# Performance work log

Measured on AMD Instinct MI355X. Metric: run time of the kernel, lower is better.

## Reference

```python
import jax, jax.numpy as jnp
import numpy as np

N = 50000      # nodes
E = 600000     # edges
D = 128        # dim_h == num_features
G = 512        # graphs in batch
BN_EPS = 1e-5


def _w(k, shape, fan_in):
    return jax.random.normal(k, shape, jnp.float32) * np.float32(1.0 / np.sqrt(fan_in))


def setup_inputs() -> dict:
    key = jax.random.key(0)
    ks = jax.random.split(key, 16)
    return {
        "x": jax.random.normal(ks[0], (N, D), jnp.float32),
        "edge_index": jax.random.randint(ks[1], (2, E), 0, N, jnp.int64),
        "batch": jnp.sort(jax.random.randint(ks[2], (N,), 0, G, jnp.int64)),
        # GINConv 1 MLP: Linear -> BN -> ReLU -> Linear -> ReLU
        "c1_W1": _w(ks[3], (D, D), D), "c1_b1": jnp.zeros((D,), jnp.float32),
        "c1_g": jnp.ones((D,), jnp.float32), "c1_be": jnp.zeros((D,), jnp.float32),
        "c1_W2": _w(ks[4], (D, D), D), "c1_b2": jnp.zeros((D,), jnp.float32),
        # GINConv 2 MLP
        "c2_W1": _w(ks[5], (D, D), D), "c2_b1": jnp.zeros((D,), jnp.float32),
        "c2_g": jnp.ones((D,), jnp.float32), "c2_be": jnp.zeros((D,), jnp.float32),
        "c2_W2": _w(ks[6], (D, D), D), "c2_b2": jnp.zeros((D,), jnp.float32),
        # readout MLP
        "lin1_W": _w(ks[7], (4 * D, 4 * D), 4 * D), "lin1_b": jnp.zeros((4 * D,), jnp.float32),
        "lin2_W": _w(ks[8], (4 * D, 1), 4 * D), "lin2_b": jnp.zeros((1,), jnp.float32),
    }


def _gin_conv(x, src, dst, W1, b1, g, be, W2, b2):
    # sum aggregation of neighbor messages (PyG GINConv, eps=0)
    agg = jax.ops.segment_sum(x[src], dst, num_segments=x.shape[0])
    h = (agg + x) @ W1 + b1
    # BatchNorm1d, training mode (biased batch stats over nodes)
    mu = h.mean(axis=0)
    var = h.var(axis=0)
    h = jax.nn.relu(g * (h - mu) * jax.lax.rsqrt(var + BN_EPS) + be)
    return jax.nn.relu(h @ W2 + b2)


def _pool(h, batch):
    add = jax.ops.segment_sum(h, batch, num_segments=G)
    mx = jax.ops.segment_max(h, batch, num_segments=G)
    mx = jnp.where(jnp.isfinite(mx), mx, 0.0)  # empty segments -> 0
    return add, mx


def reference(x, edge_index, batch,
              c1_W1, c1_b1, c1_g, c1_be, c1_W2, c1_b2,
              c2_W1, c2_b1, c2_g, c2_be, c2_W2, c2_b2,
              lin1_W, lin1_b, lin2_W, lin2_b):
    src, dst = edge_index[0], edge_index[1]
    h1 = _gin_conv(x, src, dst, c1_W1, c1_b1, c1_g, c1_be, c1_W2, c1_b2)
    h2 = _gin_conv(h1, src, dst, c2_W1, c2_b1, c2_g, c2_be, c2_W2, c2_b2)
    a1, m1 = _pool(h1, batch)
    a2, m2 = _pool(h2, batch)
    h = jnp.concatenate([a1, a2, m1, m2], axis=1)  # [G, 4D]
    h = jax.nn.relu(h @ lin1_W + lin1_b)
    h = h @ lin2_W + lin2_b  # [G, 1]
    return jax.nn.sigmoid(h), h
```

## Files before the change

### kernel.cpp

```cpp
#include <hip/hip_runtime.h>

#define D 128
#define GNUM 512

typedef _Float16 f16;
typedef _Float16 f16x2 __attribute__((ext_vector_type(2)));
typedef _Float16 f16x8 __attribute__((ext_vector_type(8)));
typedef float f32x4 __attribute__((ext_vector_type(4)));

__global__ void deg_kernel(const int* __restrict__ ei, int* __restrict__ deg,
                           int nE) {
  int e = blockIdx.x * blockDim.x + threadIdx.x;
  if (e < nE) atomicAdd(&deg[ei[nE + e]], 1);
}

__global__ __launch_bounds__(256) void partial_kernel(
    const int* __restrict__ deg, int* __restrict__ partials, int n) {
  __shared__ int sh[256];
  const int t = threadIdx.x;
  const int i = blockIdx.x * 512 + t * 2;
  int s = 0;
  if (i < n) s += deg[i];
  if (i + 1 < n) s += deg[i + 1];
  sh[t] = s;
  __syncthreads();
#pragma unroll
  for (int off = 128; off > 0; off >>= 1) {
    if (t < off) sh[t] += sh[t + off];
    __syncthreads();
  }
  if (t == 0) partials[blockIdx.x] = sh[0];
}

__global__ __launch_bounds__(128) void scanp_kernel(
    int* __restrict__ partials, int nP, int* __restrict__ rowptr, int n,
    int nE) {
  __shared__ int sh[128];
  const int t = threadIdx.x;
  const int v = (t < nP) ? partials[t] : 0;
  sh[t] = v;
  __syncthreads();
#pragma unroll
  for (int off = 1; off < 128; off <<= 1) {
    int u = (t >= off) ? sh[t - off] : 0;
    __syncthreads();
    sh[t] += u;
    __syncthreads();
  }
  if (t < nP) partials[t] = sh[t] - v;
  if (t == 0) rowptr[n] = nE;
}

__global__ __launch_bounds__(256) void emit_kernel(
    const int* __restrict__ deg, const int* __restrict__ partials,
    int* __restrict__ rowptr, int* __restrict__ cursor, int n) {
  __shared__ int sh[256];
  const int t = threadIdx.x;
  const int i = blockIdx.x * 512 + t * 2;
  const int d0 = (i < n) ? deg[i] : 0;
  const int d1 = (i + 1 < n) ? deg[i + 1] : 0;
  const int s = d0 + d1;
  sh[t] = s;
  __syncthreads();
#pragma unroll
  for (int off = 1; off < 256; off <<= 1) {
    int u = (t >= off) ? sh[t - off] : 0;
    __syncthreads();
    sh[t] += u;
    __syncthreads();
  }
  int base = partials[blockIdx.x] + sh[t] - s;
  if (i < n) {
    rowptr[i] = base;
    cursor[i] = base;
    base += d0;
  }
  if (i + 1 < n) {
    rowptr[i + 1] = base;
    cursor[i + 1] = base;
  }
}

__global__ void fill_kernel(const int* __restrict__ ei, int* __restrict__ cursor,
                            int* __restrict__ csr, int nE) {
  int e = blockIdx.x * blockDim.x + threadIdx.x;
  if (e < nE) {
    int d = ei[nE + e];
    int pos = atomicAdd(&cursor[d], 1);
    csr[pos] = ei[e];
  }
}

__global__ __launch_bounds__(256) void prep_kernel(
    const float* __restrict__ x, f16* __restrict__ x16, int n4,
    const float* __restrict__ W0, const float* __restrict__ W1,
    const float* __restrict__ W2, const float* __restrict__ W3,
    f16* __restrict__ wt, const int* __restrict__ batch,
    int* __restrict__ gstart, int n, int nxblk) {
  const int b = blockIdx.x;
  if (b < nxblk) {
    int i = b * 256 + threadIdx.x;
    if (i < n4) {
      float4 v = ((const float4*)x)[i];
      union { f16 h[4]; uint2 u; } p;
      p.h[0] = (f16)v.x; p.h[1] = (f16)v.y;
      p.h[2] = (f16)v.z; p.h[3] = (f16)v.w;
      ((uint2*)x16)[i] = p.u;
    }
  } else if (b < nxblk + 256) {
    int idx = (b - nxblk) * 256 + threadIdx.x;
    int wsel = idx >> 14;
    int rem = idx & 16383;
    int col = rem >> 7, k = rem & 127;
    const float* W = (wsel == 0) ? W0 : (wsel == 1) ? W1
                                      : (wsel == 2) ? W2 : W3;
    wt[idx] = (f16)W[k * D + col];
  } else {
    int g = (b - nxblk - 256) * 256 + threadIdx.x;
    if (g > GNUM) return;
    if (g == GNUM) { gstart[g] = n; return; }
    int lo = 0, hi = n;
    while (lo < hi) {
      int mid = (lo + hi) >> 1;
      if (batch[mid] < g) lo = mid + 1; else hi = mid;
    }
    gstart[g] = lo;
  }
}

__global__ __launch_bounds__(256) void gemmfused_kernel(
    const f16* __restrict__ feat, const int* __restrict__ rowptr,
    const int* __restrict__ csr, const f16* __restrict__ WT,
    const float* __restrict__ bias, f16* __restrict__ C,
    float* __restrict__ pstat, int n) {
  __shared__ f16 alds[32][136];
  const int t = threadIdx.x;
  const int w = t >> 6;
  const int l = t & 63;
  const int rb = blockIdx.x * 32;

  {
    const int c = l * 2;
#pragma unroll 1
    for (int rr = w * 8; rr < w * 8 + 8; rr++) {
      const int row = rb + rr;
      float a0 = 0.f, a1 = 0.f;
      if (row < n) {
        f16x2 v = *(const f16x2*)(feat + (size_t)row * D + c);
        a0 = (float)v[0]; a1 = (float)v[1];
        const int beg = rowptr[row], end = rowptr[row + 1];
        int i = beg;
        for (; i + 7 < end; i += 8) {
          int s0 = csr[i],     s1 = csr[i + 1], s2 = csr[i + 2], s3 = csr[i + 3];
          int s4 = csr[i + 4], s5 = csr[i + 5], s6 = csr[i + 6], s7 = csr[i + 7];
          f16x2 v0 = *(const f16x2*)(feat + (size_t)s0 * D + c);
          f16x2 v1 = *(const f16x2*)(feat + (size_t)s1 * D + c);
          f16x2 v2 = *(const f16x2*)(feat + (size_t)s2 * D + c);
          f16x2 v3 = *(const f16x2*)(feat + (size_t)s3 * D + c);
          f16x2 v4 = *(const f16x2*)(feat + (size_t)s4 * D + c);
          f16x2 v5 = *(const f16x2*)(feat + (size_t)s5 * D + c);
          f16x2 v6 = *(const f16x2*)(feat + (size_t)s6 * D + c);
          f16x2 v7 = *(const f16x2*)(feat + (size_t)s7 * D + c);
          a0 += ((float)v0[0] + (float)v1[0]) + ((float)v2[0] + (float)v3[0]) +
                ((float)v4[0] + (float)v5[0]) + ((float)v6[0] + (float)v7[0]);
          a1 += ((float)v0[1] + (float)v1[1]) + ((float)v2[1] + (float)v3[1]) +
                ((float)v4[1] + (float)v5[1]) + ((float)v6[1] + (float)v7[1]);
        }
        for (; i + 3 < end; i += 4) {
          int s0 = csr[i], s1 = csr[i + 1], s2 = csr[i + 2], s3 = csr[i + 3];
          f16x2 v0 = *(const f16x2*)(feat + (size_t)s0 * D + c);
          f16x2 v1 = *(const f16x2*)(feat + (size_t)s1 * D + c);
          f16x2 v2 = *(const f16x2*)(feat + (size_t)s2 * D + c);
          f16x2 v3 = *(const f16x2*)(feat + (size_t)s3 * D + c);
          a0 += (float)v0[0] + (float)v1[0] + (float)v2[0] + (float)v3[0];
          a1 += (float)v0[1] + (float)v1[1] + (float)v2[1] + (float)v3[1];
        }
        for (; i < end; i++) {
          f16x2 v = *(const f16x2*)(feat + (size_t)csr[i] * D + c);
          a0 += (float)v[0];
          a1 += (float)v[1];
        }
      }
      f16x2 o;
      o[0] = (f16)a0;
      o[1] = (f16)a1;
      *(f16x2*)(&alds[rr][c]) = o;
    }
  }
  __syncthreads();

  const int lr = l & 15;
  const int lq = l >> 4;
  const int lk = lq * 8;
  const int cb = w * 32;

  f32x4 acc[2][2];
#pragma unroll
  for (int m = 0; m < 2; m++)
#pragma unroll
    for (int nt = 0; nt < 2; nt++) acc[m][nt] = (f32x4)0.f;

#pragma unroll
  for (int s = 0; s < 4; s++) {
    const int k = s * 32 + lk;
    f16x8 af[2];
#pragma unroll
    for (int m = 0; m < 2; m++)
      af[m] = *(const f16x8*)(&alds[m * 16 + lr][k]);
    f16x8 bf[2];
#pragma unroll
    for (int nt = 0; nt < 2; nt++)
      bf[nt] = *(const f16x8*)(WT + (size_t)(cb + nt * 16 + lr) * D + k);
#pragma unroll
    for (int m = 0; m < 2; m++)
#pragma unroll
      for (int nt = 0; nt < 2; nt++)
        acc[m][nt] = __builtin_amdgcn_mfma_f32_16x16x32_f16(af[m], bf[nt],
                                                            acc[m][nt], 0, 0, 0);
  }

  float ts[2], tq[2];
#pragma unroll
  for (int nt = 0; nt < 2; nt++) { ts[nt] = 0.f; tq[nt] = 0.f; }
#pragma unroll
  for (int m = 0; m < 2; m++)
#pragma unroll
    for (int r = 0; r < 4; r++) {
      int row = rb + m * 16 + lq * 4 + r;
      if (row < n) {
#pragma unroll
        for (int nt = 0; nt < 2; nt++) {
          float v = acc[m][nt][r] + bias[cb + nt * 16 + lr];
          C[(size_t)row * D + cb + nt * 16 + lr] = (f16)v;
          ts[nt] += v;
          tq[nt] = fmaf(v, v, tq[nt]);
        }
      }
    }
#pragma unroll
  for (int nt = 0; nt < 2; nt++) {
    ts[nt] += __shfl_xor(ts[nt], 16); ts[nt] += __shfl_xor(ts[nt], 32);
    tq[nt] += __shfl_xor(tq[nt], 16); tq[nt] += __shfl_xor(tq[nt], 32);
  }
  if (l < 16) {
    float* ps = pstat + (size_t)blockIdx.x * 256;
#pragma unroll
    for (int nt = 0; nt < 2; nt++) {
      ps[cb + nt * 16 + l] = ts[nt];
      ps[128 + cb + nt * 16 + l] = tq[nt];
    }
  }
}

__global__ __launch_bounds__(64) void gemmbn_kernel(
    const f16* __restrict__ A, const float* __restrict__ ss,
    const f16* __restrict__ WT, const float* __restrict__ bias,
    f16* __restrict__ C, int n) {
  const int l = threadIdx.x;
  const int rw0 = blockIdx.x * 32;
  const int lr = l & 15;
  const int lq = l >> 4;
  const int lk = lq * 8;

  f32x4 acc[2][8];
#pragma unroll
  for (int m = 0; m < 2; m++)
#pragma unroll
    for (int nt = 0; nt < 8; nt++) acc[m][nt] = (f32x4)0.f;

#pragma unroll
  for (int s = 0; s < 4; s++) {
    const int k = s * 32 + lk;
    float4 c0 = *(const float4*)(ss + k);
    float4 c1 = *(const float4*)(ss + k + 4);
    float4 h0 = *(const float4*)(ss + 128 + k);
    float4 h1 = *(const float4*)(ss + 128 + k + 4);
    f16x8 af[2];
#pragma unroll
    for (int m = 0; m < 2; m++) {
      int row = rw0 + m * 16 + lr;
      f16x8 v = (f16x8)(f16)0.f;
      if (row < n) v = *(const f16x8*)(A + (size_t)row * D + k);
      f16x8 r;
      r[0] = (f16)fmaxf(0.f, fmaf((float)v[0], c0.x, h0.x));
      r[1] = (f16)fmaxf(0.f, fmaf((float)v[1], c0.y, h0.y));
      r[2] = (f16)fmaxf(0.f, fmaf((float)v[2], c0.z, h0.z));
      r[3] = (f16)fmaxf(0.f, fmaf((float)v[3], c0.w, h0.w));
      r[4] = (f16)fmaxf(0.f, fmaf((float)v[4], c1.x, h1.x));
      r[5] = (f16)fmaxf(0.f, fmaf((float)v[5], c1.y, h1.y));
      r[6] = (f16)fmaxf(0.f, fmaf((float)v[6], c1.z, h1.z));
      r[7] = (f16)fmaxf(0.f, fmaf((float)v[7], c1.w, h1.w));
      af[m] = r;
    }
    f16x8 bf[8];
#pragma unroll
    for (int nt = 0; nt < 8; nt++)
      bf[nt] = *(const f16x8*)(WT + (size_t)(nt * 16 + lr) * D + k);
#pragma unroll
    for (int m = 0; m < 2; m++)
#pragma unroll
      for (int nt = 0; nt < 8; nt++)
        acc[m][nt] = __builtin_amdgcn_mfma_f32_16x16x32_f16(af[m], bf[nt],
                                                            acc[m][nt], 0, 0, 0);
  }

#pragma unroll
  for (int m = 0; m < 2; m++)
#pragma unroll
    for (int r = 0; r < 4; r++) {
      int row = rw0 + m * 16 + lq * 4 + r;
      if (row < n) {
#pragma unroll
        for (int nt = 0; nt < 8; nt++) {
          float v = fmaxf(0.f, acc[m][nt][r] + bias[nt * 16 + lr]);
          C[(size_t)row * D + nt * 16 + lr] = (f16)v;
        }
      }
    }
}

__global__ __launch_bounds__(256) void statreduce_kernel(
    const float* __restrict__ pstat, float* __restrict__ pstat2, int nB) {
  int c = threadIdx.x;
  float s = 0.f;
  for (int b = blockIdx.x; b < nB; b += 32)
    s += pstat[(size_t)b * 256 + c];
  pstat2[(size_t)blockIdx.x * 256 + c] = s;
}

__global__ void bnstats_kernel(const float* __restrict__ pstat2,
                               const float* __restrict__ g,
                               const float* __restrict__ be,
                               float* __restrict__ ss, int n) {
  int c = threadIdx.x;
  float s = 0.f, sq = 0.f;
#pragma unroll
  for (int i = 0; i < 32; i++) {
    s += pstat2[i * 256 + c];
    sq += pstat2[i * 256 + 128 + c];
  }
  float inv_n = 1.0f / (float)n;
  float mean = s * inv_n;
  float var = sq * inv_n - mean * mean;
  float scale = g[c] * rsqrtf(var + 1e-5f);
  ss[c] = scale;
  ss[128 + c] = be[c] - mean * scale;
}

__global__ __launch_bounds__(512) void poolout_kernel(
    const f16* __restrict__ h1, const f16* __restrict__ h2,
    const int* __restrict__ gstart, const float* __restrict__ W1,
    const float* __restrict__ b1, const float* __restrict__ W2,
    const float* __restrict__ b2, float* __restrict__ out) {
  __shared__ float prow[2][512];
  __shared__ float shred[8][2];
  const int t = threadIdx.x;
  const int g0 = blockIdx.x * 2;
  {
    const int sub = t >> 8;
    const int src = (t >> 7) & 1;
    const int c = t & 127;
    const f16* hp = src ? h2 : h1;
    const int r0 = gstart[g0 + sub], r1 = gstart[g0 + sub + 1];
    float s = 0.f, m = 0.f;
    int r = r0;
    for (; r + 1 < r1; r += 2) {
      float a = (float)hp[(size_t)r * D + c];
      float b = (float)hp[(size_t)(r + 1) * D + c];
      s += a + b;
      m = fmaxf(m, fmaxf(a, b));
    }
    if (r < r1) {
      float a = (float)hp[(size_t)r * D + c];
      s += a;
      m = fmaxf(m, a);
    }
    prow[sub][src * 128 + c] = s;
    prow[sub][256 + src * 128 + c] = m;
  }
  __syncthreads();
  float a00 = 0.f, a01 = 0.f, a10 = 0.f, a11 = 0.f;
  for (int k = 0; k < 512; k += 2) {
    float w0 = W1[(size_t)k * 512 + t];
    float w1 = W1[(size_t)(k + 1) * 512 + t];
    a00 = fmaf(prow[0][k], w0, a00);
    a01 = fmaf(prow[0][k + 1], w1, a01);
    a10 = fmaf(prow[1][k], w0, a10);
    a11 = fmaf(prow[1][k + 1], w1, a11);
  }
  const float bj = b1[t];
  const float w2 = W2[t];
  float acc0 = fmaxf(0.f, a00 + a01 + bj) * w2;
  float acc1 = fmaxf(0.f, a10 + a11 + bj) * w2;
  const int w = t >> 6, l = t & 63;
#pragma unroll
  for (int off = 32; off > 0; off >>= 1) {
    acc0 += __shfl_down(acc0, off);
    acc1 += __shfl_down(acc1, off);
  }
  if (l == 0) {
    shred[w][0] = acc0;
    shred[w][1] = acc1;
  }
  __syncthreads();
  if (t < 2) {
    float s = 0.f;
#pragma unroll
    for (int i = 0; i < 8; i++) s += shred[i][t];
    float h = s + b2[0];
    out[g0 + t] = 1.0f / (1.0f + expf(-h));
    out[GNUM + g0 + t] = h;
  }
}

extern "C" void kernel_launch(void* const* d_in, const int* in_sizes, int n_in,
                              void* d_out, int out_size, void* d_ws,
                              size_t ws_size, hipStream_t stream) {
  const float* x = (const float*)d_in[0];
  const int* ei = (const int*)d_in[1];
  const int* batch = (const int*)d_in[2];
  const float* c1_W1 = (const float*)d_in[3];
  const float* c1_b1 = (const float*)d_in[4];
  const float* c1_g  = (const float*)d_in[5];
  const float* c1_be = (const float*)d_in[6];
  const float* c1_W2 = (const float*)d_in[7];
  const float* c1_b2 = (const float*)d_in[8];
  const float* c2_W1 = (const float*)d_in[9];
  const float* c2_b1 = (const float*)d_in[10];
  const float* c2_g  = (const float*)d_in[11];
  const float* c2_be = (const float*)d_in[12];
  const float* c2_W2 = (const float*)d_in[13];
  const float* c2_b2 = (const float*)d_in[14];
  const float* lin1_W = (const float*)d_in[15];
  const float* lin1_b = (const float*)d_in[16];
  const float* lin2_W = (const float*)d_in[17];
  const float* lin2_b = (const float*)d_in[18];

  const int n = in_sizes[0] / D;
  const int nE = in_sizes[1] / 2;

  char* p = (char*)d_ws;
  auto take = [&](size_t bytes) {
    char* r = p;
    p += (bytes + 255) & ~(size_t)255;
    return r;
  };
  f16*   hpre   = (f16*)take((size_t)n * D * 2);
  f16*   h2buf  = (f16*)take((size_t)n * D * 2);
  f16*   h1     = (f16*)take((size_t)n * D * 2);
  f16*   wt     = (f16*)take(4 * 16384 * 2);
  int*   deg    = (int*)take((size_t)n * 4);
  float* ssbuf  = (float*)take(256 * 4);
  int*   gstart = (int*)take((GNUM + 1) * 4);
  int* rowptr   = (int*)take((size_t)(n + 1) * 4);
  int* cursor   = (int*)take((size_t)(n + 1) * 4);
  int* partials = (int*)take(128 * 4);
  int* csr      = (int*)take((size_t)nE * 4);
  const int nB = (n + 31) / 32;
  float* pstat  = (float*)take((size_t)nB * 256 * 4);
  float* pstat2 = (float*)take(32 * 256 * 4);

  const int edge_grid = (nE + 255) / 256;
  const int nP = (n + 511) / 512;
  const int n4 = n * D / 4;
  const int nxblk = (n4 + 255) / 256;
  const int prep_grid = nxblk + 256 + 3;

  hipMemsetAsync(deg, 0, (size_t)n * sizeof(int), stream);
  deg_kernel<<<edge_grid, 256, 0, stream>>>(ei, deg, nE);
  partial_kernel<<<nP, 256, 0, stream>>>(deg, partials, n);
  scanp_kernel<<<1, 128, 0, stream>>>(partials, nP, rowptr, n, nE);
  emit_kernel<<<nP, 256, 0, stream>>>(deg, partials, rowptr, cursor, n);
  fill_kernel<<<edge_grid, 256, 0, stream>>>(ei, cursor, csr, nE);
  prep_kernel<<<prep_grid, 256, 0, stream>>>(x, h1, n4, c1_W1, c1_W2, c2_W1,
                                             c2_W2, wt, batch, gstart, n,
                                             nxblk);

  gemmfused_kernel<<<nB, 256, 0, stream>>>(h1, rowptr, csr, wt, c1_b1, hpre,
                                           pstat, n);
  statreduce_kernel<<<32, 256, 0, stream>>>(pstat, pstat2, nB);
  bnstats_kernel<<<1, 128, 0, stream>>>(pstat2, c1_g, c1_be, ssbuf, n);
  gemmbn_kernel<<<nB, 64, 0, stream>>>(hpre, ssbuf, wt + 16384, c1_b2, h1, n);

  gemmfused_kernel<<<nB, 256, 0, stream>>>(h1, rowptr, csr, wt + 32768, c2_b1,
                                           hpre, pstat, n);
  statreduce_kernel<<<32, 256, 0, stream>>>(pstat, pstat2, nB);
  bnstats_kernel<<<1, 128, 0, stream>>>(pstat2, c2_g, c2_be, ssbuf, n);
  gemmbn_kernel<<<nB, 64, 0, stream>>>(hpre, ssbuf, wt + 49152, c2_b2,
                                       h2buf, n);

  poolout_kernel<<<GNUM / 2, 512, 0, stream>>>(h1, h2buf, gstart, lin1_W,
                                               lin1_b, lin2_W, lin2_b,
                                               (float*)d_out);
}
```

Baseline: 254.6 us.

## Fold degree count into prep kernel and reduce BN stats with atomics

The degree-counting pass moves into the prep kernel as extra blocks, so one launch does the x conversion, weight transpose, graph starts and degree atomics. The gemmfused kernel now atomically adds its per-block column sums into 32 striped partial buffers instead of writing per-block partials. This removes the two statreduce launches and the large pstat buffer, and a single memset now zeroes deg and both stat buffers. The cost is float atomic contention and a non-deterministic summation order for the batch-norm statistics.

```diff
diff --git a/kernel.cpp b/kernel.cpp
--- a/kernel.cpp
+++ b/kernel.cpp
@@ -7,12 +7,6 @@
 typedef _Float16 f16x2 __attribute__((ext_vector_type(2)));
 typedef _Float16 f16x8 __attribute__((ext_vector_type(8)));
 typedef float f32x4 __attribute__((ext_vector_type(4)));
-
-__global__ void deg_kernel(const int* __restrict__ ei, int* __restrict__ deg,
-                           int nE) {
-  int e = blockIdx.x * blockDim.x + threadIdx.x;
-  if (e < nE) atomicAdd(&deg[ei[nE + e]], 1);
-}
 
 __global__ __launch_bounds__(256) void partial_kernel(
     const int* __restrict__ deg, int* __restrict__ partials, int n) {
@@ -96,7 +90,8 @@
     const float* __restrict__ W0, const float* __restrict__ W1,
     const float* __restrict__ W2, const float* __restrict__ W3,
     f16* __restrict__ wt, const int* __restrict__ batch,
-    int* __restrict__ gstart, int n, int nxblk) {
+    int* __restrict__ gstart, const int* __restrict__ ei,
+    int* __restrict__ deg, int nE, int n, int nxblk) {
   const int b = blockIdx.x;
   if (b < nxblk) {
     int i = b * 256 + threadIdx.x;
@@ -115,7 +110,7 @@
     const float* W = (wsel == 0) ? W0 : (wsel == 1) ? W1
                                       : (wsel == 2) ? W2 : W3;
     wt[idx] = (f16)W[k * D + col];
-  } else {
+  } else if (b < nxblk + 259) {
     int g = (b - nxblk - 256) * 256 + threadIdx.x;
     if (g > GNUM) return;
     if (g == GNUM) { gstart[g] = n; return; }
@@ -125,6 +120,9 @@
       if (batch[mid] < g) lo = mid + 1; else hi = mid;
     }
     gstart[g] = lo;
+  } else {
+    int e = (b - nxblk - 259) * 256 + threadIdx.x;
+    if (e < nE) atomicAdd(&deg[ei[nE + e]], 1);
   }
 }
 
@@ -132,7 +130,7 @@
     const f16* __restrict__ feat, const int* __restrict__ rowptr,
     const int* __restrict__ csr, const f16* __restrict__ WT,
     const float* __restrict__ bias, f16* __restrict__ C,
-    float* __restrict__ pstat, int n) {
+    float* __restrict__ pstat2, int n) {
   __shared__ f16 alds[32][136];
   const int t = threadIdx.x;
   const int w = t >> 6;
@@ -243,11 +241,11 @@
     tq[nt] += __shfl_xor(tq[nt], 16); tq[nt] += __shfl_xor(tq[nt], 32);
   }
   if (l < 16) {
-    float* ps = pstat + (size_t)blockIdx.x * 256;
+    float* ps = pstat2 + (size_t)(blockIdx.x & 31) * 256;
 #pragma unroll
     for (int nt = 0; nt < 2; nt++) {
-      ps[cb + nt * 16 + l] = ts[nt];
-      ps[128 + cb + nt * 16 + l] = tq[nt];
+      atomicAdd(ps + cb + nt * 16 + l, ts[nt]);
+      atomicAdd(ps + 128 + cb + nt * 16 + l, tq[nt]);
     }
   }
 }
@@ -317,15 +315,6 @@
         }
       }
     }
-}
-
-__global__ __launch_bounds__(256) void statreduce_kernel(
-    const float* __restrict__ pstat, float* __restrict__ pstat2, int nB) {
-  int c = threadIdx.x;
-  float s = 0.f;
-  for (int b = blockIdx.x; b < nB; b += 32)
-    s += pstat[(size_t)b * 256 + c];
-  pstat2[(size_t)blockIdx.x * 256 + c] = s;
 }
 
 __global__ void bnstats_kernel(const float* __restrict__ pstat2,
@@ -449,7 +438,10 @@
   f16*   h2buf  = (f16*)take((size_t)n * D * 2);
   f16*   h1     = (f16*)take((size_t)n * D * 2);
   f16*   wt     = (f16*)take(4 * 16384 * 2);
-  int*   deg    = (int*)take((size_t)n * 4);
+  int*   deg     = (int*)take((size_t)n * 4);
+  float* pstat2a = (float*)take(32 * 256 * 4);
+  float* pstat2b = (float*)take(32 * 256 * 4);
+  char*  zend    = p;
   float* ssbuf  = (float*)take(256 * 4);
   int*   gstart = (int*)take((GNUM + 1) * 4);
   int* rowptr   = (int*)take((size_t)(n + 1) * 4);
@@ -457,35 +449,30 @@
   int* partials = (int*)take(128 * 4);
   int* csr      = (int*)take((size_t)nE * 4);
   const int nB = (n + 31) / 32;
-  float* pstat  = (float*)take((size_t)nB * 256 * 4);
-  float* pstat2 = (float*)take(32 * 256 * 4);
 
   const int edge_grid = (nE + 255) / 256;
   const int nP = (n + 511) / 512;
   const int n4 = n * D / 4;
   const int nxblk = (n4 + 255) / 256;
-  const int prep_grid = nxblk + 256 + 3;
-
-  hipMemsetAsync(deg, 0, (size_t)n * sizeof(int), stream);
-  deg_kernel<<<edge_grid, 256, 0, stream>>>(ei, deg, nE);
+  const int prep_grid = nxblk + 259 + edge_grid;
+
+  hipMemsetAsync(deg, 0, (size_t)(zend - (char*)deg), stream);
+  prep_kernel<<<prep_grid, 256, 0, stream>>>(x, h1, n4, c1_W1, c1_W2, c2_W1,
+                                             c2_W2, wt, batch, gstart, ei,
+                                             deg, nE, n, nxblk);
   partial_kernel<<<nP, 256, 0, stream>>>(deg, partials, n);
   scanp_kernel<<<1, 128, 0, stream>>>(partials, nP, rowptr, n, nE);
   emit_kernel<<<nP, 256, 0, stream>>>(deg, partials, rowptr, cursor, n);
   fill_kernel<<<edge_grid, 256, 0, stream>>>(ei, cursor, csr, nE);
-  prep_kernel<<<prep_grid, 256, 0, stream>>>(x, h1, n4, c1_W1, c1_W2, c2_W1,
-                                             c2_W2, wt, batch, gstart, n,
-                                             nxblk);
 
   gemmfused_kernel<<<nB, 256, 0, stream>>>(h1, rowptr, csr, wt, c1_b1, hpre,
-                                           pstat, n);
-  statreduce_kernel<<<32, 256, 0, stream>>>(pstat, pstat2, nB);
-  bnstats_kernel<<<1, 128, 0, stream>>>(pstat2, c1_g, c1_be, ssbuf, n);
+                                           pstat2a, n);
+  bnstats_kernel<<<1, 128, 0, stream>>>(pstat2a, c1_g, c1_be, ssbuf, n);
   gemmbn_kernel<<<nB, 64, 0, stream>>>(hpre, ssbuf, wt + 16384, c1_b2, h1, n);
 
   gemmfused_kernel<<<nB, 256, 0, stream>>>(h1, rowptr, csr, wt + 32768, c2_b1,
-                                           hpre, pstat, n);
-  statreduce_kernel<<<32, 256, 0, stream>>>(pstat, pstat2, nB);
-  bnstats_kernel<<<1, 128, 0, stream>>>(pstat2, c2_g, c2_be, ssbuf, n);
+                                           hpre, pstat2b, n);
+  bnstats_kernel<<<1, 128, 0, stream>>>(pstat2b, c2_g, c2_be, ssbuf, n);
   gemmbn_kernel<<<nB, 64, 0, stream>>>(hpre, ssbuf, wt + 49152, c2_b2,
                                        h2buf, n);
 
```

Result: faster. 228.7 us (median of 2 runs) (-10.2%).
